# Kernel optimization log

Measured on AMD Instinct MI355X. Metric: run time of the kernel, lower is better.

The kernel has to match this reference:

```python
import jax, jax.numpy as jnp
import numpy as np

V, D, T, B, MS, WIN, EOS = 10000, 256, 128, 8, 4, 1, 4
S = MS + 1          # decoder segment length (y_input0 + MAX_SEGMENT tokens)
HRATE = 0.1
LOGINF = 1e6


def setup_inputs() -> dict:
    key = jax.random.key(0)
    ks = jax.random.split(key, 17)
    s = lambda i, shape: (jax.random.normal(ks[i], shape, jnp.float32) * 0.05)
    return dict(
        x_ids=jax.random.randint(ks[0], (B, T + 2 * WIN), 0, V),
        lens=jnp.full((B,), T, dtype=jnp.int32),
        emb=s(1, (V, D)),
        y_start=s(2, (1, D)),
        cell_Wi=s(3, (4 * D, D)), cell_Wh=s(4, (4 * D, D)), cell_b=s(5, (4 * D,)),
        yin0_W=s(6, (D, D)), yin0_b=s(7, (D,)),
        hlin_W=s(8, (2 * D, D)), hlin_b=s(9, (2 * D,)),
        l0_Wi=s(10, (4 * D, D)), l0_Wh=s(11, (4 * D, D)), l0_b=s(12, (4 * D,)),
        l1_Wi=s(13, (4 * D, D)), l1_Wh=s(14, (4 * D, D)), l1_b=s(15, (4 * D,)),
        out_b=s(16, (V,)),
    )


def _cell(x, h, c, Wi, Wh, b):
    # torch LSTM gate order: i, f, g, o
    g = x @ Wi.T + h @ Wh.T + b
    i, f, gg, o = jnp.split(g, 4, axis=-1)
    c2 = jax.nn.sigmoid(f) * c + jax.nn.sigmoid(i) * jnp.tanh(gg)
    return jax.nn.sigmoid(o) * jnp.tanh(c2), c2


def reference(x_ids, lens, emb, y_start, cell_Wi, cell_Wh, cell_b,
              yin0_W, yin0_b, hlin_W, hlin_b,
              l0_Wi, l0_Wh, l0_b, l1_Wi, l1_Wh, l1_b, out_b):
    y = x_ids[:, WIN:-WIN]                     # [B, T] target ids
    x = emb[y]                                 # [B, T, D]

    # --- encoder LSTMCell scan over j_start (state persists across schedule) ---
    seq = jnp.concatenate(
        [jnp.broadcast_to(y_start, (B, D))[None], jnp.transpose(x, (1, 0, 2))[:-1]], 0)  # [T,B,D]
    z = jnp.zeros((B, D), x.dtype)
    def enc_step(carry, xt):
        h, c = carry
        h2, c2 = _cell(xt, h, c, cell_Wi, cell_Wh, cell_b)
        return (h2, c2), h2
    _, h_seq = jax.lax.scan(enc_step, (z, z), seq)        # [T, B, D]

    drop_h = HRATE * h_seq
    y_in0 = drop_h @ yin0_W.T + yin0_b                    # [T, B, D]
    h0_all = jnp.tanh(drop_h @ hlin_W.T + hlin_b).reshape(T, B, 2, D)  # per-layer init h

    # --- build decoder inputs [T, B, S, D]: (y_input0, x[j_start:j_start+MS]) ---
    xp = jnp.pad(x, ((0, 0), (0, MS), (0, 0)))            # zero-pad time (causal => pads don't affect valid outputs)
    pos = jnp.arange(T)[:, None] + jnp.arange(MS)[None, :]           # [T, MS]
    seg_x = jnp.transpose(xp[:, pos], (1, 0, 2, 3))       # [T, B, MS, D]
    seg = jnp.concatenate([y_in0[:, :, None, :], seg_x], axis=2)     # [T, B, S, D]

    # --- 2-layer LSTM decoder, vmapped over j_start ---
    def decode(seg_t, h_init):                            # seg_t [B,S,D], h_init [B,2,D]
        def step(carry, xt):
            (h0, c0), (h1, c1) = carry
            h0n, c0n = _cell(xt, h0, c0, l0_Wi, l0_Wh, l0_b)
            h1n, c1n = _cell(h0n, h1, c1, l1_Wi, l1_Wh, l1_b)
            return ((h0n, c0n), (h1n, c1n)), h1n
        init = ((h_init[:, 0], z), (h_init[:, 1], z))
        _, hs = jax.lax.scan(step, init, jnp.transpose(seg_t, (1, 0, 2)))
        return jnp.transpose(hs, (1, 0, 2))               # [B, S, D]
    dec_h = jax.vmap(decode)(seg, h0_all)                 # [T, B, S, D]

    # --- tied output projection + log-softmax (only needed gathers kept) ---
    logits = jnp.einsum('tbsd,vd->tbsv', dec_h, emb) + out_b         # [T,B,S,V]
    logZ = jax.nn.logsumexp(logits, axis=-1)                          # [T,B,S]

    tgt = jnp.transpose(y[:, jnp.clip(pos, 0, T - 1)], (1, 0, 2))     # [T,B,MS]
    tgt_lp = jnp.take_along_axis(logits[:, :, :MS, :], tgt[..., None], axis=3)[..., 0] \
             - logZ[:, :, :MS]                                        # [T,B,MS]
    pmask = (pos < T)[:, None, :]
    cum = jnp.cumsum(jnp.where(pmask, tgt_lp, 0.0), axis=2)           # [T,B,MS]
    eos_lp = logits[:, :, 1:, EOS] - logZ[:, :, 1:]                   # [T,B,MS]

    kmask = (jnp.arange(T)[:, None] + jnp.arange(1, MS + 1)[None, :]) <= T   # [T,MS]
    body = jnp.where(kmask[:, None, :], cum + eos_lp, -LOGINF)        # [T,B,MS]
    logpy = jnp.concatenate([jnp.full((T, 1, B), -LOGINF, body.dtype),
                             jnp.transpose(body, (0, 2, 1))], axis=1)  # [T, MS+1, B]

    # --- alpha forward DP: alpha[j] = logsumexp_L alpha[j-L] + logpy[j-L][L] ---
    jj = jnp.arange(1, T + 1)[:, None]
    ii = jnp.arange(MS)[None, :]
    sstart = jj - MS + ii                                             # [T,MS]
    LPG = jnp.where((sstart >= 0)[..., None],
                    logpy[jnp.clip(sstart, 0), jnp.broadcast_to(MS - ii, (T, MS))],
                    -LOGINF)                                          # [T,MS,B]

    Apad0 = jnp.full((MS + T + 1, B), -LOGINF, logpy.dtype).at[MS].set(0.0)
    def dp_step(Apad, args):
        j, lpg = args
        win = jax.lax.dynamic_slice(Apad, (j, 0), (MS, B))            # alpha[j-MS .. j-1]
        aj = jax.nn.logsumexp(win + lpg, axis=0)
        return jax.lax.dynamic_update_slice(Apad, aj[None], (MS + j, 0)), None
    Apad, _ = jax.lax.scan(dp_step, Apad0, (jnp.arange(1, T + 1), LPG))
    alpha = Apad[MS:]                                                 # [T+1, B]

    ret = -jnp.sum(alpha[lens, jnp.arange(B)]) / jnp.sum(lens).astype(alpha.dtype)
    return ret
```

## Files before the change

### kernel.cpp

```cpp
#include <hip/hip_runtime.h>

#define V_ 10000
#define D_ 256
#define T_ 128
#define B_ 8
#define MS_ 4
#define S_ 5
#define EOS_ 4

typedef unsigned short b16_t;
typedef __attribute__((ext_vector_type(8))) short s16x8;
typedef __attribute__((ext_vector_type(8))) unsigned short u16x8;
typedef __attribute__((ext_vector_type(4))) float f32x4;
typedef __attribute__((ext_vector_type(2))) _Float16 h16x2;

__device__ inline b16_t f2bf(float f) {
  union { float f; unsigned u; } v; v.f = f;
  unsigned r = v.u + 0x7FFFu + ((v.u >> 16) & 1u);
  return (b16_t)(r >> 16);
}
__device__ inline float bf2f(b16_t h) {
  union { unsigned u; float f; } v; v.u = ((unsigned)h) << 16; return v.f;
}
__device__ inline float sigm_(float x) { return 1.0f / (1.0f + __expf(-x)); }
__device__ inline float tanh_(float x) { return 2.0f / (1.0f + __expf(-2.0f * x)) - 1.0f; }
__device__ inline h16x2 bch(unsigned u) { return __builtin_bit_cast(h16x2, u); }
__device__ inline unsigned pkh(float a, float b) {
  h16x2 v; v.x = (_Float16)a; v.y = (_Float16)b;
  return __builtin_bit_cast(unsigned, v);
}

#if __has_builtin(__builtin_amdgcn_fdot2)
#define FDOT2(a, b, c) __builtin_amdgcn_fdot2((a), (b), (c), false)
#else
#define FDOT2(a, b, c) ((c) + (float)(a).x * (float)(b).x + (float)(a).y * (float)(b).y)
#endif

__device__ inline float qswap1(float x) {
  return __builtin_bit_cast(float, __builtin_amdgcn_update_dpp(
      0, __builtin_bit_cast(int, x), 0xB1, 0xF, 0xF, true));
}

__device__ inline void cvt4(const float* __restrict__ s, b16_t* __restrict__ d) {
  float4 v = *(const float4*)s;
  ushort4 o = { f2bf(v.x), f2bf(v.y), f2bf(v.z), f2bf(v.w) };
  *(ushort4*)d = o;
}

__global__ __launch_bounds__(256) void k_prep(
    const float* __restrict__ emb, const float* __restrict__ cWi,
    const float* __restrict__ y0W, const float* __restrict__ hlW,
    const float* __restrict__ l0Wi, const float* __restrict__ l0Wh,
    const float* __restrict__ l1Wi, const float* __restrict__ l1Wh,
    const float* __restrict__ cWh, const int* __restrict__ x_ids,
    const float* __restrict__ y_st, const float* __restrict__ cb,
    b16_t* __restrict__ emb_bf,
    b16_t* __restrict__ y0W_bf, b16_t* __restrict__ hlW_bf,
    b16_t* __restrict__ l0Wi_bf, b16_t* __restrict__ l0Wh_bf,
    b16_t* __restrict__ Wcat_bf, unsigned* __restrict__ Whf,
    b16_t* __restrict__ seg_bf, float* __restrict__ encX) {
  int blk = blockIdx.x;
  int tid = threadIdx.x;
  if (blk < 1024) {
    for (long i = (long)blk * 256 + tid; i < 1278976L; i += 1024L * 256) {
      if (i < 640000L) { cvt4(emb + i * 4, emb_bf + i * 4); }
      else if (i < 656384L) { long j = i - 640000L; cvt4(y0W + j * 4, y0W_bf + j * 4); }
      else if (i < 689152L) { long j = i - 656384L; cvt4(hlW + j * 4, hlW_bf + j * 4); }
      else if (i < 754688L) { long j = i - 689152L; cvt4(l0Wi + j * 4, l0Wi_bf + j * 4); }
      else if (i < 820224L) { long j = i - 754688L; cvt4(l0Wh + j * 4, l0Wh_bf + j * 4); }
      else if (i < 951296L) {
        long j = (i - 820224L) * 4;
        long n = j >> 9; int k = (int)(j & 511);
        const float* src = (k < 256) ? (l1Wi + n * 256 + k) : (l1Wh + n * 256 + (k - 256));
        cvt4(src, Wcat_bf + j);
      } else if (i < 1016832L) {
        long j = i - 951296L;
        float4 v = *(const float4*)(cWh + j * 4);
        Whf[2 * j] = pkh(v.x, v.y);
        Whf[2 * j + 1] = pkh(v.z, v.w);
      } else {
        long j = i - 1016832L;
        int r = (int)(j >> 6), c = (int)(j & 63) * 4;
        int p = r >> 2, s = 1 + (r & 3);
        int t = p >> 3, b = p & 7;
        int tt = t + s - 1;
        int ps = r + (r >> 2) + 1;
        if (tt < T_) {
          int tok = x_ids[b * (T_ + 2) + tt + 1];
          cvt4(emb + (size_t)tok * D_ + c, seg_bf + (size_t)ps * 256 + c);
        } else {
          ushort4 z = {0, 0, 0, 0};
          *(ushort4*)(seg_bf + (size_t)ps * 256 + c) = z;
        }
      }
    }
  } else {
    __shared__ b16_t As[64][264];
    __shared__ b16_t Bs[64][264];
    int bx2 = blk - 1024;
    int rb = (bx2 >> 4) * 64, colBase = (bx2 & 15) * 64;
    for (int i = tid; i < 64 * 32; i += 256) {
      int r = i >> 5, c = (i & 31) * 8;
      int m = rb + r;
      int t = m >> 3, b = m & 7;
      const float* asrc = (t == 0) ? (y_st + c)
                                   : (emb + (size_t)x_ids[b * (T_ + 2) + t] * D_ + c);
      cvt4(asrc, &As[r][c]);
      cvt4(asrc + 4, &As[r][c + 4]);
      const float* bsrc = cWi + (size_t)(colBase + r) * 256 + c;
      cvt4(bsrc, &Bs[r][c]);
      cvt4(bsrc + 4, &Bs[r][c + 4]);
    }
    __syncthreads();
    int w = tid >> 6, l = tid & 63, lr = l & 15, kg = l >> 4;
    f32x4 acc[4] = {{0.f,0.f,0.f,0.f},{0.f,0.f,0.f,0.f},{0.f,0.f,0.f,0.f},{0.f,0.f,0.f,0.f}};
    for (int kk = 0; kk < 8; ++kk) {
      s16x8 a = *(const s16x8*)&As[w * 16 + lr][kk * 32 + kg * 8];
#pragma unroll
      for (int f = 0; f < 4; ++f) {
        s16x8 b = *(const s16x8*)&Bs[f * 16 + lr][kk * 32 + kg * 8];
        acc[f] = __builtin_amdgcn_mfma_f32_16x16x32_bf16(a, b, acc[f], 0, 0, 0);
      }
    }
#pragma unroll
    for (int f = 0; f < 4; ++f) {
#pragma unroll
      for (int r = 0; r < 4; ++r) {
        int m = rb + w * 16 + kg * 4 + r;
        int n = colBase + f * 16 + lr;
        encX[(size_t)m * 1024 + n] = acc[f][r] + cb[n];
      }
    }
  }
}

#define ENC_CH4(i0)                                                            \
  do {                                                                         \
    uint4 a0 = hp[i0], a1 = hp[i0 + 1], a2 = hp[i0 + 2], a3 = hp[i0 + 3];      \
    s0 = FDOT2(bch(a0.x), bch(wv[4 * (i0) + 0]), s0);                          \
    s1 = FDOT2(bch(a0.y), bch(wv[4 * (i0) + 1]), s1);                          \
    s0 = FDOT2(bch(a0.z), bch(wv[4 * (i0) + 2]), s0);                          \
    s1 = FDOT2(bch(a0.w), bch(wv[4 * (i0) + 3]), s1);                          \
    s0 = FDOT2(bch(a1.x), bch(wv[4 * (i0) + 4]), s0);                          \
    s1 = FDOT2(bch(a1.y), bch(wv[4 * (i0) + 5]), s1);                          \
    s0 = FDOT2(bch(a1.z), bch(wv[4 * (i0) + 6]), s0);                          \
    s1 = FDOT2(bch(a1.w), bch(wv[4 * (i0) + 7]), s1);                          \
    s0 = FDOT2(bch(a2.x), bch(wv[4 * (i0) + 8]), s0);                          \
    s1 = FDOT2(bch(a2.y), bch(wv[4 * (i0) + 9]), s1);                          \
    s0 = FDOT2(bch(a2.z), bch(wv[4 * (i0) + 10]), s0);                         \
    s1 = FDOT2(bch(a2.w), bch(wv[4 * (i0) + 11]), s1);                         \
    s0 = FDOT2(bch(a3.x), bch(wv[4 * (i0) + 12]), s0);                         \
    s1 = FDOT2(bch(a3.y), bch(wv[4 * (i0) + 13]), s1);                         \
    s0 = FDOT2(bch(a3.z), bch(wv[4 * (i0) + 14]), s0);                         \
    s1 = FDOT2(bch(a3.w), bch(wv[4 * (i0) + 15]), s1);                         \
  } while (0)

struct EncS { unsigned hbuf[128]; float gl[256]; };
struct GemS { b16_t As[64][264]; b16_t Bs[64][264]; };

__global__ __launch_bounds__(512, 2) void k_enc_x0(
    const unsigned* __restrict__ Whf,
    const float* __restrict__ encX,
    unsigned* __restrict__ hglob,
    b16_t* __restrict__ droph,
    const b16_t* __restrict__ seg_bf, const b16_t* __restrict__ l0Wi_bf,
    const float* __restrict__ l0b, float* __restrict__ X0) {
  __shared__ union { EncS e; GemS g; } sm;
  int tid = threadIdx.x;
  if (blockIdx.x < 32) {
    int b = blockIdx.x & 7, q = blockIdx.x >> 3;
    int r = tid >> 1, ch = tid & 1;
    int growr = ((r >> 6) << 8) + q * 64 + (r & 63);
    unsigned wv[64];
    {
      const uint4* wp = (const uint4*)(Whf + (size_t)growr * 128 + ch * 64);
#pragma unroll
      for (int i = 0; i < 16; ++i) {
        uint4 v = wp[i];
        wv[4*i] = v.x; wv[4*i+1] = v.y; wv[4*i+2] = v.z; wv[4*i+3] = v.w;
      }
    }
#pragma unroll
    for (int i = 0; i < 64; ++i) asm volatile("" : "+v"(wv[i]));
    if (tid < 128) sm.e.hbuf[tid] = 0;
    float c = 0.f;
    float ex = encX[(size_t)b * 1024 + growr];
    __syncthreads();
#pragma unroll 1
    for (int t = 0; t < 128; ++t) {
      const uint4* hp = (const uint4*)&sm.e.hbuf[ch * 64];
      float s0 = 0.f, s1 = 0.f;
      ENC_CH4(0);
      __builtin_amdgcn_sched_barrier(0);
      ENC_CH4(4);
      __builtin_amdgcn_sched_barrier(0);
      ENC_CH4(8);
      __builtin_amdgcn_sched_barrier(0);
      ENC_CH4(12);
      float sum = s0 + s1;
      sum += qswap1(sum);
      if (ch == 0) sm.e.gl[r] = sum + ex;
      __syncthreads();
      if (tid < 64) {
        float gi = sm.e.gl[tid], gf = sm.e.gl[64 + tid];
        float gg = sm.e.gl[128 + tid], go = sm.e.gl[192 + tid];
        float c2 = sigm_(gf) * c + sigm_(gi) * tanh_(gg);
        float h2 = sigm_(go) * tanh_(c2);
        c = c2;
        float hnb = qswap1(h2);
        if ((tid & 1) == 0) {
          unsigned pk = pkh(h2, hnb) | 0x00010001u;
          sm.e.hbuf[q * 32 + (tid >> 1)] = pk;
          if (t < 127)
            __hip_atomic_store(&hglob[(((size_t)t * 8 + b) * 4 + q) * 32 + (tid >> 1)],
                               pk, __ATOMIC_RELAXED, __HIP_MEMORY_SCOPE_AGENT);
        }
        droph[((size_t)t * 8 + b) * 256 + q * 64 + tid] = f2bf(0.1f * h2);
      }
      if (t < 127) {
        if (tid >= 64 && tid < 160) {
          int idx = tid - 64;
          int ro = idx >> 5;
          int rq = ro + (ro >= q);
          int dw = idx & 31;
          unsigned* src = &hglob[(((size_t)t * 8 + b) * 4 + rq) * 32 + dw];
          unsigned v;
          do {
            v = __hip_atomic_load(src, __ATOMIC_RELAXED, __HIP_MEMORY_SCOPE_AGENT);
          } while (v == 0u);
          sm.e.hbuf[rq * 32 + dw] = v;
        }
        ex = encX[((size_t)(t + 1) * 8 + b) * 1024 + growr];
        __syncthreads();
      }
    }
  } else {
    int bx2 = blockIdx.x - 32;
    int rb = (bx2 & 63) * 64;
    int colBase = (bx2 >> 6) * 64;
    if (tid < 256) {
      for (int i = tid; i < 64 * 32; i += 256) {
        int r = i >> 5, cc = (i & 31) * 8;
        int jj = rb + r, ps = jj + (jj >> 2) + 1;
        *(u16x8*)&sm.g.As[r][cc] = *(const u16x8*)(seg_bf + (size_t)ps * 256 + cc);
        *(u16x8*)&sm.g.Bs[r][cc] = *(const u16x8*)(l0Wi_bf + (size_t)(colBase + r) * 256 + cc);
      }
    }
    __syncthreads();
    if (tid < 256) {
      int w = tid >> 6, l = tid & 63, lr = l & 15, kg = l >> 4;
      f32x4 acc[4] = {{0.f,0.f,0.f,0.f},{0.f,0.f,0.f,0.f},{0.f,0.f,0.f,0.f},{0.f,0.f,0.f,0.f}};
      for (int kk = 0; kk < 8; ++kk) {
        s16x8 a = *(const s16x8*)&sm.g.As[w * 16 + lr][kk * 32 + kg * 8];
#pragma unroll
        for (int f = 0; f < 4; ++f) {
          s16x8 b = *(const s16x8*)&sm.g.Bs[f * 16 + lr][kk * 32 + kg * 8];
          acc[f] = __builtin_amdgcn_mfma_f32_16x16x32_bf16(a, b, acc[f], 0, 0, 0);
        }
      }
#pragma unroll
      for (int f = 0; f < 4; ++f) {
#pragma unroll
        for (int r = 0; r < 4; ++r) {
          int jj = rb + w * 16 + kg * 4 + r;
          int ps = jj + (jj >> 2) + 1;
          int n = colBase + f * 16 + lr;
          X0[(size_t)ps * 1024 + n] = acc[f][r] + l0b[n];
        }
      }
    }
  }
}

__global__ __launch_bounds__(256) void k_proj(
    const b16_t* __restrict__ droph, const b16_t* __restrict__ y0W_bf,
    const float* __restrict__ y0b, const b16_t* __restrict__ hlW_bf,
    const float* __restrict__ hlb, b16_t* __restrict__ seg_bf,
    b16_t* __restrict__ hcat,
    const b16_t* __restrict__ l0Wi_bf, const float* __restrict__ l0b,
    float* __restrict__ X0) {
  __shared__ b16_t As[64][264];
  __shared__ b16_t Bs[64][264];
  int bx = blockIdx.x, by = blockIdx.y;
  const b16_t* Ab; int lda;
  const b16_t* Bw; const float* bias; int colBase, mode;
  if (by < 4)       { Ab = droph;  lda = 256;  Bw = y0W_bf;  bias = y0b; colBase = by * 64;        mode = 0; }
  else if (by < 12) { Ab = droph;  lda = 256;  Bw = hlW_bf;  bias = hlb; colBase = (by - 4) * 64;  mode = 1; }
  else              { Ab = seg_bf; lda = 1280; Bw = l0Wi_bf; bias = l0b; colBase = (by - 12) * 64; mode = 2; }
  int rowBase = bx * 64;
  int tid = threadIdx.x;
  for (int i = tid; i < 64 * 32; i += 256) {
    int r = i >> 5, c = (i & 31) * 8;
    *(u16x8*)&As[r][c] = *(const u16x8*)(Ab + (size_t)(rowBase + r) * lda + c);
    *(u16x8*)&Bs[r][c] = *(const u16x8*)(Bw + (size_t)(colBase + r) * 256 + c);
  }
  __syncthreads();
  int w = tid >> 6, l = tid & 63, lr = l & 15, kg = l >> 4;
  f32x4 acc[4] = {{0.f,0.f,0.f,0.f},{0.f,0.f,0.f,0.f},{0.f,0.f,0.f,0.f},{0.f,0.f,0.f,0.f}};
  for (int kk = 0; kk < 8; ++kk) {
    s16x8 a = *(const s16x8*)&As[w * 16 + lr][kk * 32 + kg * 8];
#pragma unroll
    for (int f = 0; f < 4; ++f) {
      s16x8 b = *(const s16x8*)&Bs[f * 16 + lr][kk * 32 + kg * 8];
      acc[f] = __builtin_amdgcn_mfma_f32_16x16x32_bf16(a, b, acc[f], 0, 0, 0);
    }
  }
#pragma unroll
  for (int f = 0; f < 4; ++f) {
#pragma unroll
    for (int r = 0; r < 4; ++r) {
      int m = rowBase + w * 16 + kg * 4 + r;
      int n = colBase + f * 16 + lr;
      float v = acc[f][r] + bias[n];
      if (mode == 0) seg_bf[(size_t)m * 1280 + n] = f2bf(v);
      else if (mode == 1) hcat[(size_t)m * 512 + n] = f2bf(tanh_(v));
      else X0[(size_t)m * 5120 + n] = v;
    }
  }
}

__global__ __launch_bounds__(512) void k_dec2(
    b16_t* __restrict__ hcat,
    const b16_t* __restrict__ l0Wh_bf,
    const b16_t* __restrict__ Wcat_bf,
    const float* __restrict__ X0,
    const float* __restrict__ l1b,
    float* __restrict__ c0, float* __restrict__ c1,
    b16_t* __restrict__ dec_out, int s) {
  __shared__ b16_t A0s[16][264];
  __shared__ b16_t A1s[16][520];
  int tid = threadIdx.x;
  int R0 = blockIdx.x * 16;
  for (int i = tid; i < 16 * 32; i += 512) {
    int r = i >> 5, cc = (i & 31) * 8;
    *(u16x8*)&A0s[r][cc] = *(const u16x8*)(hcat + (size_t)(R0 + r) * 512 + cc);
    *(u16x8*)&A1s[r][256 + cc] = *(const u16x8*)(hcat + (size_t)(R0 + r) * 512 + 256 + cc);
  }
  __syncthreads();
  int w = tid >> 6, l = tid & 63, lr = l & 15, kg = l >> 4;
  {
    s16x8 af[8];
#pragma unroll
    for (int kk = 0; kk < 8; ++kk)
      af[kk] = *(const s16x8*)&A0s[lr][kk * 32 + kg * 8];
    f32x4 acc[4][2];
#pragma unroll
    for (int g = 0; g < 4; ++g)
#pragma unroll
      for (int ct = 0; ct < 2; ++ct) acc[g][ct] = f32x4{0.f, 0.f, 0.f, 0.f};
#pragma unroll
    for (int g = 0; g < 4; ++g)
#pragma unroll
      for (int ct = 0; ct < 2; ++ct) {
        int n = g * 256 + w * 32 + ct * 16 + lr;
        const b16_t* bp = l0Wh_bf + (size_t)n * 256 + kg * 8;
#pragma unroll
        for (int kk = 0; kk < 8; ++kk)
          acc[g][ct] = __builtin_amdgcn_mfma_f32_16x16x32_bf16(
              af[kk], *(const s16x8*)(bp + kk * 32), acc[g][ct], 0, 0, 0);
      }
#pragma unroll
    for (int ct = 0; ct < 2; ++ct)
#pragma unroll
      for (int r = 0; r < 4; ++r) {
        int row = kg * 4 + r, p = R0 + row, d = w * 32 + ct * 16 + lr;
        const float* xp = X0 + ((size_t)p * 5 + s) * 1024;
        float gi = acc[0][ct][r] + xp[d],       gf = acc[1][ct][r] + xp[256 + d];
        float gg = acc[2][ct][r] + xp[512 + d], go = acc[3][ct][r] + xp[768 + d];
        float cc0 = c0[(size_t)p * 256 + d];
        float c2 = sigm_(gf) * cc0 + sigm_(gi) * tanh_(gg);
        float h2 = sigm_(go) * tanh_(c2);
        c0[(size_t)p * 256 + d] = c2;
        b16_t hb = f2bf(h2);
        A1s[row][d] = hb;
        hcat[(size_t)p * 512 + d] = hb;
      }
  }
  __syncthreads();
  {
    s16x8 a1[16];
#pragma unroll
    for (int kk = 0; kk < 16; ++kk)
      a1[kk] = *(const s16x8*)&A1s[lr][kk * 32 + kg * 8];
    f32x4 acc[4][2];
#pragma unroll
    for (int g = 0; g < 4; ++g)
#pragma unroll
      for (int ct = 0; ct < 2; ++ct) acc[g][ct] = f32x4{0.f, 0.f, 0.f, 0.f};
#pragma unroll
    for (int g = 0; g < 4; ++g)
#pragma unroll
      for (int ct = 0; ct < 2; ++ct) {
        int n = g * 256 + w * 32 + ct * 16 + lr;
        const b16_t* bp = Wcat_bf + (size_t)n * 512 + kg * 8;
#pragma unroll
        for (int kk = 0; kk < 16; ++kk)
          acc[g][ct] = __builtin_amdgcn_mfma_f32_16x16x32_bf16(
              a1[kk], *(const s16x8*)(bp + kk * 32), acc[g][ct], 0, 0, 0);
      }
#pragma unroll
    for (int ct = 0; ct < 2; ++ct)
#pragma unroll
      for (int r = 0; r < 4; ++r) {
        int row = kg * 4 + r, p = R0 + row, d = w * 32 + ct * 16 + lr;
        float gi = acc[0][ct][r] + l1b[d],       gf = acc[1][ct][r] + l1b[256 + d];
        float gg = acc[2][ct][r] + l1b[512 + d], go = acc[3][ct][r] + l1b[768 + d];
        float cc1 = c1[(size_t)p * 256 + d];
        float c2 = sigm_(gf) * cc1 + sigm_(gi) * tanh_(gg);
        float h2 = sigm_(go) * tanh_(c2);
        c1[(size_t)p * 256 + d] = c2;
        b16_t hb = f2bf(h2);
        hcat[(size_t)p * 512 + 256 + d] = hb;
        dec_out[((size_t)p * 5 + s) * 256 + d] = hb;
      }
  }
}

__global__ __launch_bounds__(512) void k_logits_ext(
    const b16_t* __restrict__ Abf, const b16_t* __restrict__ emb_bf,
    const float* __restrict__ out_b, float* __restrict__ sumexp,
    const int* __restrict__ x_ids, float* __restrict__ tl,
    float* __restrict__ el) {
  int bid = blockIdx.x;
  int tid = threadIdx.x;
  if (bid < 240) {
    __shared__ b16_t Bs[64][264];
    int rowBase = (bid % 40) * 128;
    int w = tid >> 6, l = tid & 63, lr = l & 15, kg = l >> 4;
    s16x8 af[8];
    {
      const b16_t* arow = Abf + (size_t)(rowBase + w * 16 + lr) * 256;
#pragma unroll
      for (int kk = 0; kk < 8; ++kk) af[kk] = *(const s16x8*)(arow + kk * 32 + kg * 8);
    }
    float runsum[4] = {0.f, 0.f, 0.f, 0.f};
    int t0 = (bid / 40) * 27, t1 = (t0 + 27 < 157) ? (t0 + 27) : 157;
    for (int tile = t0; tile < t1; ++tile) {
      int colBase = tile * 64;
      __syncthreads();
      for (int i = tid; i < 64 * 32; i += 512) {
        int r = i >> 5, cc = (i & 31) * 8;
        int vrow = colBase + r;
        u16x8 bv = {0, 0, 0, 0, 0, 0, 0, 0};
        if (vrow < V_) bv = *(const u16x8*)(emb_bf + (size_t)vrow * D_ + cc);
        *(u16x8*)&Bs[r][cc] = bv;
      }
      __syncthreads();
      f32x4 acc[4] = {{0.f,0.f,0.f,0.f},{0.f,0.f,0.f,0.f},{0.f,0.f,0.f,0.f},{0.f,0.f,0.f,0.f}};
#pragma unroll
      for (int kk = 0; kk < 8; ++kk) {
#pragma unroll
        for (int f = 0; f < 4; ++f) {
          s16x8 b = *(const s16x8*)&Bs[f * 16 + lr][kk * 32 + kg * 8];
          acc[f] = __builtin_amdgcn_mfma_f32_16x16x32_bf16(af[kk], b, acc[f], 0, 0, 0);
        }
      }
#pragma unroll
      for (int f = 0; f < 4; ++f) {
        int n = colBase + f * 16 + lr;
        if (n < V_) {
          float ob = out_b[n];
#pragma unroll
          for (int r = 0; r < 4; ++r) runsum[r] += __expf(acc[f][r] + ob);
        }
      }
    }
#pragma unroll
    for (int r = 0; r < 4; ++r) {
      float rs = runsum[r];
      rs += __shfl_xor(rs, 1, 64);
      rs += __shfl_xor(rs, 2, 64);
      rs += __shfl_xor(rs, 4, 64);
      rs += __shfl_xor(rs, 8, 64);
      if (lr == 0) atomicAdd(&sumexp[rowBase + w * 16 + kg * 4 + r], rs);
    }
  } else {
    int wave = tid >> 6, lane = tid & 63;
    for (int i = 0; i < 8; ++i) {
      int p = (bid - 240) * 64 + wave * 8 + i;
      int t = p >> 3, b = p & 7;
      for (int s = 0; s < S_; ++s) {
        const b16_t* hr = Abf + ((size_t)p * S_ + s) * D_;
        float hv[4];
#pragma unroll
        for (int j = 0; j < 4; ++j) hv[j] = bf2f(hr[lane * 4 + j]);
        if (s < MS_) {
          int pos = t + s; if (pos > T_ - 1) pos = T_ - 1;
          int tok = x_ids[b * (T_ + 2) + pos + 1];
          const b16_t* er = emb_bf + (size_t)tok * D_;
          float ps = 0.f;
#pragma unroll
          for (int j = 0; j < 4; ++j) ps += hv[j] * bf2f(er[lane * 4 + j]);
          for (int m = 1; m < 64; m <<= 1) ps += __shfl_xor(ps, m, 64);
          if (lane == 0) tl[p * MS_ + s] = ps + out_b[tok];
        }
        if (s >= 1) {
          const b16_t* er = emb_bf + (size_t)EOS_ * D_;
          float ps = 0.f;
#pragma unroll
          for (int j = 0; j < 4; ++j) ps += hv[j] * bf2f(er[lane * 4 + j]);
          for (int m = 1; m < 64; m <<= 1) ps += __shfl_xor(ps, m, 64);
          if (lane == 0) el[p * MS_ + (s - 1)] = ps + out_b[EOS_];
        }
      }
    }
  }
}

__global__ __launch_bounds__(256) void k_final(const float* __restrict__ sumexp,
                                               const float* __restrict__ tl,
                                               const float* __restrict__ el,
                                               const int* __restrict__ lens,
                                               float* __restrict__ out) {
  __shared__ float logpy[T_][S_][B_];
  __shared__ float alpha[T_ + 1][B_];
  int tid = threadIdx.x;
  for (int p = tid; p < T_ * B_; p += 256) {
    int t = p >> 3, b = p & 7;
    float lz[S_];
#pragma unroll
    for (int s = 0; s < S_; ++s) lz[s] = __logf(sumexp[p * S_ + s]);
    float cum = 0.f, cums[MS_];
#pragma unroll
    for (int s = 0; s < MS_; ++s) {
      float tlp = tl[p * MS_ + s] - lz[s];
      if (t + s < T_) cum += tlp;
      cums[s] = cum;
    }
#pragma unroll
    for (int k = 1; k <= MS_; ++k) {
      float bv = -1000000.0f;
      if (t + k <= T_) bv = cums[k - 1] + (el[p * MS_ + (k - 1)] - lz[k]);
      logpy[t][k][b] = bv;
    }
  }
  __syncthreads();
  if (tid < B_) {
    int b = tid;
    alpha[0][b] = 0.f;
    for (int j = 1; j <= T_; ++j) {
      float vs[MS_], vmax = -1e30f;
#pragma unroll
      for (int k = 1; k <= MS_; ++k) {
        float vv = -2000000.0f;
        if (j - k >= 0) vv = alpha[j - k][b] + logpy[j - k][k][b];
        vs[k - 1] = vv;
        if (vv > vmax) vmax = vv;
      }
      float ssum = 0.f;
#pragma unroll
      for (int k = 0; k < MS_; ++k) ssum += __expf(vs[k] - vmax);
      alpha[j][b] = vmax + __logf(ssum);
    }
  }
  __syncthreads();
  if (tid == 0) {
    float num = 0.f, den = 0.f;
    for (int b = 0; b < B_; ++b) { num += alpha[lens[b]][b]; den += (float)lens[b]; }
    out[0] = -num / den;
  }
}

extern "C" void kernel_launch(void* const* d_in, const int* in_sizes, int n_in,
                              void* d_out, int out_size, void* d_ws, size_t ws_size,
                              hipStream_t stream) {
  const int* x_ids   = (const int*)d_in[0];
  const int* lens    = (const int*)d_in[1];
  const float* emb   = (const float*)d_in[2];
  const float* y_st  = (const float*)d_in[3];
  const float* cWi   = (const float*)d_in[4];
  const float* cWh   = (const float*)d_in[5];
  const float* cb    = (const float*)d_in[6];
  const float* y0W   = (const float*)d_in[7];
  const float* y0b   = (const float*)d_in[8];
  const float* hlW   = (const float*)d_in[9];
  const float* hlb   = (const float*)d_in[10];
  const float* l0Wi  = (const float*)d_in[11];
  const float* l0Wh  = (const float*)d_in[12];
  const float* l0b   = (const float*)d_in[13];
  const float* l1Wi  = (const float*)d_in[14];
  const float* l1Wh  = (const float*)d_in[15];
  const float* l1b   = (const float*)d_in[16];
  const float* outb  = (const float*)d_in[17];
  float* out = (float*)d_out;
  (void)in_sizes; (void)n_in; (void)out_size; (void)ws_size;

  char* ws = (char*)d_ws;
  size_t cur = 0;
  auto alloc = [&](size_t bytes) { size_t o = cur; cur += (bytes + 255) & ~(size_t)255; return o; };
  b16_t* emb_bf    = (b16_t*)(ws + alloc((size_t)V_ * D_ * 2));
  b16_t* y0W_bf    = (b16_t*)(ws + alloc(256 * 256 * 2));
  b16_t* hlW_bf    = (b16_t*)(ws + alloc(512 * 256 * 2));
  b16_t* l0Wi_bf   = (b16_t*)(ws + alloc(1024 * 256 * 2));
  b16_t* l0Wh_bf   = (b16_t*)(ws + alloc(1024 * 256 * 2));
  b16_t* Wcat_bf   = (b16_t*)(ws + alloc(1024 * 512 * 2));
  unsigned* Whf    = (unsigned*)(ws + alloc(1024 * 128 * 4));
  float* encX      = (float*)(ws + alloc((size_t)1024 * 1024 * 4));
  b16_t* droph_bf  = (b16_t*)(ws + alloc(1024 * 256 * 2));
  b16_t* hcat      = (b16_t*)(ws + alloc(1024 * 512 * 2));
  b16_t* seg_bf    = (b16_t*)(ws + alloc((size_t)5120 * 256 * 2));
  float* X0        = (float*)(ws + alloc((size_t)5120 * 1024 * 4));
  float* c0        = (float*)(ws + alloc((size_t)2 * 1024 * 256 * 4));
  float* c1        = c0 + 1024 * 256;
  b16_t* dec_h_bf  = (b16_t*)(ws + alloc((size_t)5120 * 256 * 2));
  float* sumexp    = (float*)(ws + alloc(5120 * 4));
  unsigned* hglob  = (unsigned*)(ws + alloc((size_t)128 * 8 * 4 * 32 * 4));
  float* tl        = (float*)(ws + alloc(1024 * MS_ * 4));
  float* el        = (float*)(ws + alloc(1024 * MS_ * 4));

  hipMemsetAsync(sumexp, 0, 20480 + 524288, stream);
  hipMemsetAsync(c0, 0, (size_t)2 * 1024 * 256 * 4, stream);

  k_prep<<<1280, 256, 0, stream>>>(emb, cWi, y0W, hlW, l0Wi, l0Wh, l1Wi, l1Wh, cWh,
                                   x_ids, y_st, cb,
                                   emb_bf, y0W_bf, hlW_bf, l0Wi_bf, l0Wh_bf,
                                   Wcat_bf, Whf, seg_bf, encX);

  k_enc_x0<<<1056, 512, 0, stream>>>(Whf, encX, hglob, droph_bf,
                                     seg_bf, l0Wi_bf, l0b, X0);

  k_proj<<<dim3(16, 28), 256, 0, stream>>>(droph_bf, y0W_bf, y0b, hlW_bf, hlb,
                                           seg_bf, hcat, l0Wi_bf, l0b, X0);

  for (int s = 0; s < S_; ++s)
    k_dec2<<<64, 512, 0, stream>>>(hcat, l0Wh_bf, Wcat_bf, X0, l1b, c0, c1, dec_h_bf, s);

  k_logits_ext<<<256, 512, 0, stream>>>(dec_h_bf, emb_bf, outb, sumexp,
                                        x_ids, tl, el);
  k_final<<<1, 256, 0, stream>>>(sumexp, tl, el, lens, out);
}
```

Baseline: 567.8 us.

## Overlap vocab logsumexp of previous decoder step with current LSTM step

Merges the decoder step kernel with the vocabulary logits/sum-exp kernel. Blocks 0-63 run the two-layer LSTM step s, while 192 extra blocks compute the sum-exp over the vocabulary for the outputs of step s-1. A final kernel handles step 4's logits plus the target/EOS dot products. The aim is to fill idle CUs during the latency-bound decoder steps and shrink the standalone logits kernel, in exchange for more launch blocks per step and a changed sumexp indexing layout.

```diff
diff --git a/kernel.cpp b/kernel.cpp
--- a/kernel.cpp
+++ b/kernel.cpp
@@ -319,122 +319,119 @@
   }
 }
 
-__global__ __launch_bounds__(512) void k_dec2(
+__global__ __launch_bounds__(512) void k_declog(
     b16_t* __restrict__ hcat,
     const b16_t* __restrict__ l0Wh_bf,
     const b16_t* __restrict__ Wcat_bf,
     const float* __restrict__ X0,
     const float* __restrict__ l1b,
     float* __restrict__ c0, float* __restrict__ c1,
-    b16_t* __restrict__ dec_out, int s) {
-  __shared__ b16_t A0s[16][264];
-  __shared__ b16_t A1s[16][520];
+    b16_t* __restrict__ dec_out,
+    const b16_t* __restrict__ emb_bf, const float* __restrict__ out_b,
+    float* __restrict__ sumexp, int s) {
   int tid = threadIdx.x;
-  int R0 = blockIdx.x * 16;
-  for (int i = tid; i < 16 * 32; i += 512) {
-    int r = i >> 5, cc = (i & 31) * 8;
-    *(u16x8*)&A0s[r][cc] = *(const u16x8*)(hcat + (size_t)(R0 + r) * 512 + cc);
-    *(u16x8*)&A1s[r][256 + cc] = *(const u16x8*)(hcat + (size_t)(R0 + r) * 512 + 256 + cc);
-  }
-  __syncthreads();
-  int w = tid >> 6, l = tid & 63, lr = l & 15, kg = l >> 4;
-  {
-    s16x8 af[8];
-#pragma unroll
-    for (int kk = 0; kk < 8; ++kk)
-      af[kk] = *(const s16x8*)&A0s[lr][kk * 32 + kg * 8];
-    f32x4 acc[4][2];
-#pragma unroll
-    for (int g = 0; g < 4; ++g)
-#pragma unroll
-      for (int ct = 0; ct < 2; ++ct) acc[g][ct] = f32x4{0.f, 0.f, 0.f, 0.f};
-#pragma unroll
-    for (int g = 0; g < 4; ++g)
-#pragma unroll
-      for (int ct = 0; ct < 2; ++ct) {
-        int n = g * 256 + w * 32 + ct * 16 + lr;
-        const b16_t* bp = l0Wh_bf + (size_t)n * 256 + kg * 8;
-#pragma unroll
-        for (int kk = 0; kk < 8; ++kk)
-          acc[g][ct] = __builtin_amdgcn_mfma_f32_16x16x32_bf16(
-              af[kk], *(const s16x8*)(bp + kk * 32), acc[g][ct], 0, 0, 0);
-      }
-#pragma unroll
-    for (int ct = 0; ct < 2; ++ct)
-#pragma unroll
-      for (int r = 0; r < 4; ++r) {
-        int row = kg * 4 + r, p = R0 + row, d = w * 32 + ct * 16 + lr;
-        const float* xp = X0 + ((size_t)p * 5 + s) * 1024;
-        float gi = acc[0][ct][r] + xp[d],       gf = acc[1][ct][r] + xp[256 + d];
-        float gg = acc[2][ct][r] + xp[512 + d], go = acc[3][ct][r] + xp[768 + d];
-        float cc0 = c0[(size_t)p * 256 + d];
-        float c2 = sigm_(gf) * cc0 + sigm_(gi) * tanh_(gg);
-        float h2 = sigm_(go) * tanh_(c2);
-        c0[(size_t)p * 256 + d] = c2;
-        b16_t hb = f2bf(h2);
-        A1s[row][d] = hb;
-        hcat[(size_t)p * 512 + d] = hb;
-      }
-  }
-  __syncthreads();
-  {
-    s16x8 a1[16];
-#pragma unroll
-    for (int kk = 0; kk < 16; ++kk)
-      a1[kk] = *(const s16x8*)&A1s[lr][kk * 32 + kg * 8];
-    f32x4 acc[4][2];
-#pragma unroll
-    for (int g = 0; g < 4; ++g)
-#pragma unroll
-      for (int ct = 0; ct < 2; ++ct) acc[g][ct] = f32x4{0.f, 0.f, 0.f, 0.f};
-#pragma unroll
-    for (int g = 0; g < 4; ++g)
-#pragma unroll
-      for (int ct = 0; ct < 2; ++ct) {
-        int n = g * 256 + w * 32 + ct * 16 + lr;
-        const b16_t* bp = Wcat_bf + (size_t)n * 512 + kg * 8;
-#pragma unroll
-        for (int kk = 0; kk < 16; ++kk)
-          acc[g][ct] = __builtin_amdgcn_mfma_f32_16x16x32_bf16(
-              a1[kk], *(const s16x8*)(bp + kk * 32), acc[g][ct], 0, 0, 0);
-      }
-#pragma unroll
-    for (int ct = 0; ct < 2; ++ct)
-#pragma unroll
-      for (int r = 0; r < 4; ++r) {
-        int row = kg * 4 + r, p = R0 + row, d = w * 32 + ct * 16 + lr;
-        float gi = acc[0][ct][r] + l1b[d],       gf = acc[1][ct][r] + l1b[256 + d];
-        float gg = acc[2][ct][r] + l1b[512 + d], go = acc[3][ct][r] + l1b[768 + d];
-        float cc1 = c1[(size_t)p * 256 + d];
-        float c2 = sigm_(gf) * cc1 + sigm_(gi) * tanh_(gg);
-        float h2 = sigm_(go) * tanh_(c2);
-        c1[(size_t)p * 256 + d] = c2;
-        b16_t hb = f2bf(h2);
-        hcat[(size_t)p * 512 + 256 + d] = hb;
-        dec_out[((size_t)p * 5 + s) * 256 + d] = hb;
-      }
-  }
-}
-
-__global__ __launch_bounds__(512) void k_logits_ext(
-    const b16_t* __restrict__ Abf, const b16_t* __restrict__ emb_bf,
-    const float* __restrict__ out_b, float* __restrict__ sumexp,
-    const int* __restrict__ x_ids, float* __restrict__ tl,
-    float* __restrict__ el) {
-  int bid = blockIdx.x;
-  int tid = threadIdx.x;
-  if (bid < 240) {
+  if (blockIdx.x < 64) {
+    __shared__ b16_t A0s[16][264];
+    __shared__ b16_t A1s[16][520];
+    int R0 = blockIdx.x * 16;
+    for (int i = tid; i < 16 * 32; i += 512) {
+      int r = i >> 5, cc = (i & 31) * 8;
+      *(u16x8*)&A0s[r][cc] = *(const u16x8*)(hcat + (size_t)(R0 + r) * 512 + cc);
+      *(u16x8*)&A1s[r][256 + cc] = *(const u16x8*)(hcat + (size_t)(R0 + r) * 512 + 256 + cc);
+    }
+    __syncthreads();
+    int w = tid >> 6, l = tid & 63, lr = l & 15, kg = l >> 4;
+    {
+      s16x8 af[8];
+#pragma unroll
+      for (int kk = 0; kk < 8; ++kk)
+        af[kk] = *(const s16x8*)&A0s[lr][kk * 32 + kg * 8];
+      f32x4 acc[4][2];
+#pragma unroll
+      for (int g = 0; g < 4; ++g)
+#pragma unroll
+        for (int ct = 0; ct < 2; ++ct) acc[g][ct] = f32x4{0.f, 0.f, 0.f, 0.f};
+#pragma unroll
+      for (int g = 0; g < 4; ++g)
+#pragma unroll
+        for (int ct = 0; ct < 2; ++ct) {
+          int n = g * 256 + w * 32 + ct * 16 + lr;
+          const b16_t* bp = l0Wh_bf + (size_t)n * 256 + kg * 8;
+#pragma unroll
+          for (int kk = 0; kk < 8; ++kk)
+            acc[g][ct] = __builtin_amdgcn_mfma_f32_16x16x32_bf16(
+                af[kk], *(const s16x8*)(bp + kk * 32), acc[g][ct], 0, 0, 0);
+        }
+#pragma unroll
+      for (int ct = 0; ct < 2; ++ct)
+#pragma unroll
+        for (int r = 0; r < 4; ++r) {
+          int row = kg * 4 + r, p = R0 + row, d = w * 32 + ct * 16 + lr;
+          const float* xp = X0 + ((size_t)p * 5 + s) * 1024;
+          float gi = acc[0][ct][r] + xp[d],       gf = acc[1][ct][r] + xp[256 + d];
+          float gg = acc[2][ct][r] + xp[512 + d], go = acc[3][ct][r] + xp[768 + d];
+          float cc0 = c0[(size_t)p * 256 + d];
+          float c2 = sigm_(gf) * cc0 + sigm_(gi) * tanh_(gg);
+          float h2 = sigm_(go) * tanh_(c2);
+          c0[(size_t)p * 256 + d] = c2;
+          b16_t hb = f2bf(h2);
+          A1s[row][d] = hb;
+          hcat[(size_t)p * 512 + d] = hb;
+        }
+    }
+    __syncthreads();
+    {
+      s16x8 a1[16];
+#pragma unroll
+      for (int kk = 0; kk < 16; ++kk)
+        a1[kk] = *(const s16x8*)&A1s[lr][kk * 32 + kg * 8];
+      f32x4 acc[4][2];
+#pragma unroll
+      for (int g = 0; g < 4; ++g)
+#pragma unroll
+        for (int ct = 0; ct < 2; ++ct) acc[g][ct] = f32x4{0.f, 0.f, 0.f, 0.f};
+#pragma unroll
+      for (int g = 0; g < 4; ++g)
+#pragma unroll
+        for (int ct = 0; ct < 2; ++ct) {
+          int n = g * 256 + w * 32 + ct * 16 + lr;
+          const b16_t* bp = Wcat_bf + (size_t)n * 512 + kg * 8;
+#pragma unroll
+          for (int kk = 0; kk < 16; ++kk)
+            acc[g][ct] = __builtin_amdgcn_mfma_f32_16x16x32_bf16(
+                a1[kk], *(const s16x8*)(bp + kk * 32), acc[g][ct], 0, 0, 0);
+        }
+#pragma unroll
+      for (int ct = 0; ct < 2; ++ct)
+#pragma unroll
+        for (int r = 0; r < 4; ++r) {
+          int row = kg * 4 + r, p = R0 + row, d = w * 32 + ct * 16 + lr;
+          float gi = acc[0][ct][r] + l1b[d],       gf = acc[1][ct][r] + l1b[256 + d];
+          float gg = acc[2][ct][r] + l1b[512 + d], go = acc[3][ct][r] + l1b[768 + d];
+          float cc1 = c1[(size_t)p * 256 + d];
+          float c2 = sigm_(gf) * cc1 + sigm_(gi) * tanh_(gg);
+          float h2 = sigm_(go) * tanh_(c2);
+          c1[(size_t)p * 256 + d] = c2;
+          b16_t hb = f2bf(h2);
+          hcat[(size_t)p * 512 + 256 + d] = hb;
+          dec_out[((size_t)p * 5 + s) * 256 + d] = hb;
+        }
+    }
+  } else if (s > 0) {
     __shared__ b16_t Bs[64][264];
-    int rowBase = (bid % 40) * 128;
+    int bx2 = blockIdx.x - 64;
+    int prow0 = (bx2 & 7) * 128;
+    int chunk = bx2 >> 3;
+    int sl = s - 1;
     int w = tid >> 6, l = tid & 63, lr = l & 15, kg = l >> 4;
     s16x8 af[8];
     {
-      const b16_t* arow = Abf + (size_t)(rowBase + w * 16 + lr) * 256;
+      const b16_t* arow = dec_out + (((size_t)(prow0 + w * 16 + lr)) * 5 + sl) * 256;
 #pragma unroll
       for (int kk = 0; kk < 8; ++kk) af[kk] = *(const s16x8*)(arow + kk * 32 + kg * 8);
     }
     float runsum[4] = {0.f, 0.f, 0.f, 0.f};
-    int t0 = (bid / 40) * 27, t1 = (t0 + 27 < 157) ? (t0 + 27) : 157;
+    int t0 = chunk * 7, t1 = (t0 + 7 < 157) ? (t0 + 7) : 157;
     for (int tile = t0; tile < t1; ++tile) {
       int colBase = tile * 64;
       __syncthreads();
@@ -472,15 +469,83 @@
       rs += __shfl_xor(rs, 2, 64);
       rs += __shfl_xor(rs, 4, 64);
       rs += __shfl_xor(rs, 8, 64);
-      if (lr == 0) atomicAdd(&sumexp[rowBase + w * 16 + kg * 4 + r], rs);
+      if (lr == 0) {
+        int p = prow0 + w * 16 + kg * 4 + r;
+        atomicAdd(&sumexp[p * 5 + sl], rs);
+      }
+    }
+  }
+}
+
+__global__ __launch_bounds__(512) void k_last(
+    const b16_t* __restrict__ dec_out, const b16_t* __restrict__ emb_bf,
+    const float* __restrict__ out_b, float* __restrict__ sumexp,
+    const int* __restrict__ x_ids, float* __restrict__ tl,
+    float* __restrict__ el) {
+  int bid = blockIdx.x;
+  int tid = threadIdx.x;
+  if (bid < 192) {
+    __shared__ b16_t Bs[64][264];
+    int prow0 = (bid & 7) * 128;
+    int chunk = bid >> 3;
+    int w = tid >> 6, l = tid & 63, lr = l & 15, kg = l >> 4;
+    s16x8 af[8];
+    {
+      const b16_t* arow = dec_out + (((size_t)(prow0 + w * 16 + lr)) * 5 + 4) * 256;
+#pragma unroll
+      for (int kk = 0; kk < 8; ++kk) af[kk] = *(const s16x8*)(arow + kk * 32 + kg * 8);
+    }
+    float runsum[4] = {0.f, 0.f, 0.f, 0.f};
+    int t0 = chunk * 7, t1 = (t0 + 7 < 157) ? (t0 + 7) : 157;
+    for (int tile = t0; tile < t1; ++tile) {
+      int colBase = tile * 64;
+      __syncthreads();
+      for (int i = tid; i < 64 * 32; i += 512) {
+        int r = i >> 5, cc = (i & 31) * 8;
+        int vrow = colBase + r;
+        u16x8 bv = {0, 0, 0, 0, 0, 0, 0, 0};
+        if (vrow < V_) bv = *(const u16x8*)(emb_bf + (size_t)vrow * D_ + cc);
+        *(u16x8*)&Bs[r][cc] = bv;
+      }
+      __syncthreads();
+      f32x4 acc[4] = {{0.f,0.f,0.f,0.f},{0.f,0.f,0.f,0.f},{0.f,0.f,0.f,0.f},{0.f,0.f,0.f,0.f}};
+#pragma unroll
+      for (int kk = 0; kk < 8; ++kk) {
+#pragma unroll
+        for (int f = 0; f < 4; ++f) {
+          s16x8 b = *(const s16x8*)&Bs[f * 16 + lr][kk * 32 + kg * 8];
+          acc[f] = __builtin_amdgcn_mfma_f32_16x16x32_bf16(af[kk], b, acc[f], 0, 0, 0);
+        }
+      }
+#pragma unroll
+      for (int f = 0; f < 4; ++f) {
+        int n = colBase + f * 16 + lr;
+        if (n < V_) {
+          float ob = out_b[n];
+#pragma unroll
+          for (int r = 0; r < 4; ++r) runsum[r] += __expf(acc[f][r] + ob);
+        }
+      }
+    }
+#pragma unroll
+    for (int r = 0; r < 4; ++r) {
+      float rs = runsum[r];
+      rs += __shfl_xor(rs, 1, 64);
+      rs += __shfl_xor(rs, 2, 64);
+      rs += __shfl_xor(rs, 4, 64);
+      rs += __shfl_xor(rs, 8, 64);
+      if (lr == 0) {
+        int p = prow0 + w * 16 + kg * 4 + r;
+        atomicAdd(&sumexp[p * 5 + 4], rs);
+      }
     }
   } else {
     int wave = tid >> 6, lane = tid & 63;
     for (int i = 0; i < 8; ++i) {
-      int p = (bid - 240) * 64 + wave * 8 + i;
+      int p = (bid - 192) * 64 + wave * 8 + i;
       int t = p >> 3, b = p & 7;
       for (int s = 0; s < S_; ++s) {
-        const b16_t* hr = Abf + ((size_t)p * S_ + s) * D_;
+        const b16_t* hr = dec_out + ((size_t)p * S_ + s) * D_;
         float hv[4];
 #pragma unroll
         for (int j = 0; j < 4; ++j) hv[j] = bf2f(hr[lane * 4 + j]);
@@ -623,9 +688,9 @@
                                            seg_bf, hcat, l0Wi_bf, l0b, X0);
 
   for (int s = 0; s < S_; ++s)
-    k_dec2<<<64, 512, 0, stream>>>(hcat, l0Wh_bf, Wcat_bf, X0, l1b, c0, c1, dec_h_bf, s);
-
-  k_logits_ext<<<256, 512, 0, stream>>>(dec_h_bf, emb_bf, outb, sumexp,
-                                        x_ids, tl, el);
+    k_declog<<<256, 512, 0, stream>>>(hcat, l0Wh_bf, Wcat_bf, X0, l1b, c0, c1,
+                                      dec_h_bf, emb_bf, outb, sumexp, s);
+
+  k_last<<<208, 512, 0, stream>>>(dec_h_bf, emb_bf, outb, sumexp, x_ids, tl, el);
   k_final<<<1, 256, 0, stream>>>(sumexp, tl, el, lens, out);
 }
```

Result: no change. 571.7 us (+0.7%).
